# Performance work log

Measured on AMD Instinct MI355X. Metric: run time of the kernel, lower is better.

The kernel has to match this reference:

```python
import jax, jax.numpy as jnp
import numpy as np


def _conv1x1(x, w, b):
    # x: [B,C,H,W], w: [O,C], b: [O] -> [B,O,H,W]
    return jnp.einsum('oc,bchw->bohw', w, x) + b[None, :, None, None]


def setup_inputs() -> dict:
    key = jax.random.key(0)
    ks = jax.random.split(key, 9)
    B, C, O, H, W = 8, 192, 96, 64, 64
    s_in = 1.0 / np.sqrt(C)
    s_out = 1.0 / np.sqrt(O)
    return {
        'x': jax.random.normal(ks[0], (B, C, H, W), dtype=jnp.float32),
        'g_w': jax.random.normal(ks[1], (O, C), dtype=jnp.float32) * s_in,
        'g_b': jax.random.normal(ks[2], (O,), dtype=jnp.float32) * s_in,
        'theta_w': jax.random.normal(ks[3], (O, C), dtype=jnp.float32) * s_in,
        'theta_b': jax.random.normal(ks[4], (O,), dtype=jnp.float32) * s_in,
        'phi_w': jax.random.normal(ks[5], (O, C), dtype=jnp.float32) * s_in,
        'phi_b': jax.random.normal(ks[6], (O,), dtype=jnp.float32) * s_in,
        'W_w': jax.random.normal(ks[7], (C, O), dtype=jnp.float32) * s_out,
        'W_b': jax.random.normal(ks[8], (C,), dtype=jnp.float32) * s_out,
    }


def reference(x, g_w, g_b, theta_w, theta_b, phi_w, phi_b, W_w, W_b):
    B, C, H, W = x.shape
    O = g_w.shape[0]
    N = H * W
    # 1x1 conv projections, flattened to [B, O, N]
    g_x = _conv1x1(x, g_w, g_b).reshape(B, O, N)          # [B,O,N]
    theta_x = _conv1x1(x, theta_w, theta_b).reshape(B, O, N)
    phi_x = _conv1x1(x, phi_w, phi_b).reshape(B, O, N)
    # scores f1[b,n,m] = theta[:, :, n] . phi[:, :, m]
    f1 = jnp.einsum('bon,bom->bnm', theta_x, phi_x)       # [B,N,N]
    f_div_C = jax.nn.softmax(f1, axis=-1)
    # y[b,n,o] = sum_m f[b,n,m] * g[b,o,m]
    y = jnp.einsum('bnm,bom->bon', f_div_C, g_x)          # [B,O,N]
    y = y.reshape(B, O, H, W)
    W_y = _conv1x1(y, W_w, W_b)                           # [B,C,H,W]
    return W_y + x
```

## Files before the change

kernel.cpp:

```cpp
#include <hip/hip_runtime.h>

typedef unsigned short u16;
typedef unsigned int u32;
typedef float f32x4 __attribute__((ext_vector_type(4)));
typedef float f32x16 __attribute__((ext_vector_type(16)));
typedef _Float16 h16x8 __attribute__((ext_vector_type(8)));
typedef u32 u32x4 __attribute__((ext_vector_type(4)));
typedef u32 u32x2 __attribute__((ext_vector_type(2)));
typedef u16 u16x4 __attribute__((ext_vector_type(4)));

#define NB 8
#define CC 192
#define OO 96
#define NN 4096
#define NSPLIT 4
#define XPAD 200
#define LOG2E 1.4426950408889634f

static __device__ __forceinline__ u16 f2h(float f) {
  _Float16 h = (_Float16)f;
  return __builtin_bit_cast(u16, h);
}
static __device__ __forceinline__ void gl_lds16(const u16* g, u16* l) {
  __builtin_amdgcn_global_load_lds(
      (const __attribute__((address_space(1))) void*)g,
      (__attribute__((address_space(3))) void*)l, 16, 0, 0);
}
static __device__ __forceinline__ float exp2_raw(float x) {
  float r;
  asm("v_exp_f32 %0, %1" : "=v"(r) : "v"(x));
  return r;
}
static __device__ __forceinline__ void plane_swap(u32& a, u32& b) {
  u32x2 r = __builtin_amdgcn_permlane32_swap(a, b, false, false);
  a = r[0]; b = r[1];
}
static __device__ __forceinline__ float half_combine_max(float x) {
  u32 a = __builtin_bit_cast(u32, x), b = a;
  plane_swap(a, b);
  return fmaxf(__builtin_bit_cast(float, a), __builtin_bit_cast(float, b));
}
static __device__ __forceinline__ float half_combine_sum(float x) {
  u32 a = __builtin_bit_cast(u32, x), b = a;
  plane_swap(a, b);
  return __builtin_bit_cast(float, a) + __builtin_bit_cast(float, b);
}
static __device__ __forceinline__ float max3f(float a, float b, float c) {
  return fmaxf(fmaxf(a, b), c);
}

__global__ __launch_bounds__(256) void proj_kernel(
    const float* __restrict__ x,
    const float* __restrict__ g_w, const float* __restrict__ g_b,
    const float* __restrict__ th_w, const float* __restrict__ th_b,
    const float* __restrict__ ph_w, const float* __restrict__ ph_b,
    u16* __restrict__ QB, u16* __restrict__ KA, u16* __restrict__ VA)
{
  __shared__ __align__(16) u16 Xs[64][XPAD];
  __shared__ __align__(16) u16 Ws[96][XPAD];
  const int b = blockIdx.y, n0 = blockIdx.x * 64, tid = threadIdx.x;
  const int lane = tid & 63, wv = tid >> 6, l15 = lane & 15, lg = lane >> 4;

  #pragma unroll
  for (int it = 0; it < 12; ++it) {
    int idx = tid + it * 256;
    int c = idx >> 4, q = idx & 15;
    float4 v = *(const float4*)(x + ((size_t)(b * CC + c)) * NN + n0 + q * 4);
    Xs[q * 4 + 0][c] = f2h(v.x); Xs[q * 4 + 1][c] = f2h(v.y);
    Xs[q * 4 + 2][c] = f2h(v.z); Xs[q * 4 + 3][c] = f2h(v.w);
  }

  for (int p = 0; p < 3; ++p) {
    const float* w    = (p == 0) ? th_w : (p == 1) ? ph_w : g_w;
    const float* bias = (p == 0) ? th_b : (p == 1) ? ph_b : g_b;
    const float scale = (p == 0) ? LOG2E : 1.0f;
    __syncthreads();
    #pragma unroll
    for (int it = 0; it < 18; ++it) {
      int idx = tid + it * 256;
      int r = idx / 48, q = idx % 48;
      float4 v = *(const float4*)(w + r * CC + q * 4);
      u16x4 hh; hh[0] = f2h(v.x * scale); hh[1] = f2h(v.y * scale);
      hh[2] = f2h(v.z * scale); hh[3] = f2h(v.w * scale);
      *(u16x4*)&Ws[r][q * 4] = hh;
    }
    __syncthreads();

    f32x4 acc[6];
    #pragma unroll
    for (int of = 0; of < 6; ++of) acc[of] = (f32x4){0.f, 0.f, 0.f, 0.f};
    #pragma unroll
    for (int ks = 0; ks < 6; ++ks) {
      h16x8 xa = *(const h16x8*)&Xs[wv * 16 + l15][ks * 32 + lg * 8];
      #pragma unroll
      for (int of = 0; of < 6; ++of) {
        h16x8 wf = *(const h16x8*)&Ws[of * 16 + l15][ks * 32 + lg * 8];
        if (p < 2) acc[of] = __builtin_amdgcn_mfma_f32_16x16x32_f16(xa, wf, acc[of], 0, 0, 0);
        else       acc[of] = __builtin_amdgcn_mfma_f32_16x16x32_f16(wf, xa, acc[of], 0, 0, 0);
      }
    }

    if (p < 2) {
      u16* dst = (p == 0) ? QB : KA;
      #pragma unroll
      for (int of = 0; of < 6; ++of) {
        int o = of * 16 + l15;
        float bo = bias[o] * scale;
        int kch = of * 2 + (l15 >> 3);
        #pragma unroll
        for (int r = 0; r < 4; ++r) {
          int n = n0 + wv * 16 + lg * 4 + r;
          int idx = (b * 128 + (n >> 5)) * 3072 + (kch * 32 + (n & 31)) * 8 + (o & 7);
          dst[idx] = f2h(acc[of][r] + bo);
        }
      }
    } else {
      #pragma unroll
      for (int of = 0; of < 6; ++of) {
        #pragma unroll
        for (int r = 0; r < 4; ++r) {
          int o = of * 16 + lg * 4 + r;
          int m = n0 + wv * 16 + l15;
          int idx = (b * 256 + (m >> 4)) * 1536 +
                    (((o >> 5) * 2 + ((m >> 3) & 1)) * 32 + (o & 31)) * 8 + (m & 7);
          VA[idx] = f2h(acc[of][r] + bias[o]);
        }
      }
    }
  }
}

static __device__ __forceinline__ void qk_pair(
    const u16* kc, const h16x8* qfA, const h16x8* qfB, int h, int l31,
    f32x16& SA, f32x16& SB)
{
  #pragma unroll
  for (int i = 0; i < 16; ++i) { SA[i] = 0.f; SB[i] = 0.f; }
  #pragma unroll
  for (int ks = 0; ks < 6; ++ks) {
    h16x8 kf = *(const h16x8*)(kc + ((ks * 2 + h) * 32 + l31) * 8);
    SA = __builtin_amdgcn_mfma_f32_32x32x16_f16(kf, qfA[ks], SA, 0, 0, 0);
    SB = __builtin_amdgcn_mfma_f32_32x32x16_f16(kf, qfB[ks], SB, 0, 0, 0);
  }
}

static __device__ __forceinline__ void sm_pair(
    f32x16 SA, f32x16 SB,
    float& mA, float& lA, f32x16* accA,
    float& mB, float& lB, f32x16* accB,
    h16x8* pfA, h16x8* pfB)
{
  float a0 = max3f(SA[0], SA[1], SA[2]),  a1 = max3f(SA[3], SA[4], SA[5]);
  float a2 = max3f(SA[6], SA[7], SA[8]),  a3 = max3f(SA[9], SA[10], SA[11]);
  float a4 = max3f(SA[12], SA[13], SA[14]);
  float pmaxA = half_combine_max(fmaxf(max3f(a0, a1, a2), max3f(a3, a4, SA[15])));
  float b0 = max3f(SB[0], SB[1], SB[2]),  b1 = max3f(SB[3], SB[4], SB[5]);
  float b2 = max3f(SB[6], SB[7], SB[8]),  b3 = max3f(SB[9], SB[10], SB[11]);
  float b4 = max3f(SB[12], SB[13], SB[14]);
  float pmaxB = half_combine_max(fmaxf(max3f(b0, b1, b2), max3f(b3, b4, SB[15])));
  if (__ballot((pmaxA > mA + 11.5416f) || (pmaxB > mB + 11.5416f))) {
    float mnA = fmaxf(mA, pmaxA), scA = exp2_raw(mA - mnA);
    float mnB = fmaxf(mB, pmaxB), scB = exp2_raw(mB - mnB);
    mA = mnA; lA *= scA;
    mB = mnB; lB *= scB;
    #pragma unroll
    for (int ob = 0; ob < 3; ++ob)
      #pragma unroll
      for (int i = 0; i < 16; ++i) { accA[ob][i] *= scA; accB[ob][i] *= scB; }
  }
  #pragma unroll
  for (int i = 0; i < 16; ++i) { SA[i] = exp2_raw(SA[i] - mA); SB[i] = exp2_raw(SB[i] - mB); }
  u32 pkA[8], pkB[8];
  #pragma unroll
  for (int i = 0; i < 8; ++i) {
    pkA[i] = __builtin_bit_cast(u32, __builtin_amdgcn_cvt_pkrtz(SA[2 * i], SA[2 * i + 1]));
    pkB[i] = __builtin_bit_cast(u32, __builtin_amdgcn_cvt_pkrtz(SB[2 * i], SB[2 * i + 1]));
  }
  #pragma unroll
  for (int st = 8; st >= 1; st >>= 1)
    #pragma unroll
    for (int i = 0; i < 8; ++i)
      if (i < st) { SA[i] += SA[i + st]; SB[i] += SB[i + st]; }
  lA += half_combine_sum(SA[0]);
  lB += half_combine_sum(SB[0]);
  plane_swap(pkA[0], pkA[2]); plane_swap(pkA[1], pkA[3]);
  plane_swap(pkA[4], pkA[6]); plane_swap(pkA[5], pkA[7]);
  plane_swap(pkB[0], pkB[2]); plane_swap(pkB[1], pkB[3]);
  plane_swap(pkB[4], pkB[6]); plane_swap(pkB[5], pkB[7]);
  u32x4 a0v = {pkA[0], pkA[1], pkA[2], pkA[3]}, a1v = {pkA[4], pkA[5], pkA[6], pkA[7]};
  u32x4 b0v = {pkB[0], pkB[1], pkB[2], pkB[3]}, b1v = {pkB[4], pkB[5], pkB[6], pkB[7]};
  pfA[0] = __builtin_bit_cast(h16x8, a0v); pfA[1] = __builtin_bit_cast(h16x8, a1v);
  pfB[0] = __builtin_bit_cast(h16x8, b0v); pfB[1] = __builtin_bit_cast(h16x8, b1v);
}

static __device__ __forceinline__ void pv_pair(
    const u16* vc, const h16x8* pfA, const h16x8* pfB, int h, int l31,
    f32x16* accA, f32x16* accB)
{
  #pragma unroll
  for (int s2 = 0; s2 < 2; ++s2) {
    #pragma unroll
    for (int ob = 0; ob < 3; ++ob) {
      h16x8 vf = *(const h16x8*)(vc + (((s2 * 3 + ob) * 2 + h) * 32 + l31) * 8);
      accA[ob] = __builtin_amdgcn_mfma_f32_32x32x16_f16(vf, pfA[s2], accA[ob], 0, 0, 0);
      accB[ob] = __builtin_amdgcn_mfma_f32_32x32x16_f16(vf, pfB[s2], accB[ob], 0, 0, 0);
    }
  }
}

__global__ __launch_bounds__(128, 2) void attn_kernel(
    const u16* __restrict__ QB, const u16* __restrict__ KA,
    const u16* __restrict__ VA, u16* __restrict__ yP, float* __restrict__ ml)
{
  __shared__ __align__(16) u16 Ks[6144];
  __shared__ __align__(16) u16 Vs[6144];
  const int b   = blockIdx.x;
  const int qt  = blockIdx.y;
  const int sp  = blockIdx.z;
  const int tid = threadIdx.x;
  const int lane = tid & 63;
  const int wv  = tid >> 6;
  const int l31 = lane & 31;
  const int h   = lane >> 5;

  const int t_start = 16 * sp;
  const int t_end   = 16 * (sp + 1);

  const int ncA = qt * 4 + wv * 2;
  const int ncB = ncA + 1;
  const u16* qbA = QB + (size_t)(b * 128 + ncA) * 3072;
  const u16* qbB = QB + (size_t)(b * 128 + ncB) * 3072;
  h16x8 qfA[6], qfB[6];
  #pragma unroll
  for (int ks = 0; ks < 6; ++ks) {
    qfA[ks] = *(const h16x8*)(qbA + ((ks * 2 + h) * 32 + l31) * 8);
    qfB[ks] = *(const h16x8*)(qbB + ((ks * 2 + h) * 32 + l31) * 8);
  }

  const u16* gk = KA + (size_t)b * (128 * 3072) + (size_t)t_start * 6144;
  const u16* gv = VA + (size_t)b * (256 * 1536) + (size_t)t_start * 6144;

  f32x16 accA[3], accB[3];
  #pragma unroll
  for (int ob = 0; ob < 3; ++ob)
    #pragma unroll
    for (int i = 0; i < 16; ++i) { accA[ob][i] = 0.f; accB[ob][i] = 0.f; }
  float mA = -3.0e38f, lA = 0.f;
  float mB = -3.0e38f, lB = 0.f;

  for (int t = t_start; t < t_end; ++t) {
    #pragma unroll
    for (int i = 0; i < 6; ++i) gl_lds16(gk + tid * 8 + i * 1024, &Ks[tid * 8 + i * 1024]);
    #pragma unroll
    for (int i = 0; i < 6; ++i) gl_lds16(gv + tid * 8 + i * 1024, &Vs[tid * 8 + i * 1024]);
    gk += 6144; gv += 6144;
    asm volatile("s_waitcnt vmcnt(0)" ::: "memory");
    __builtin_amdgcn_s_barrier();
    __builtin_amdgcn_sched_barrier(0);

    f32x16 SA0, SB0, SA1, SB1;
    h16x8 pfA[2], pfB[2];
    qk_pair(&Ks[0],    qfA, qfB, h, l31, SA0, SB0);
    qk_pair(&Ks[3072], qfA, qfB, h, l31, SA1, SB1);
    sm_pair(SA0, SB0, mA, lA, accA, mB, lB, accB, pfA, pfB);
    pv_pair(&Vs[0], pfA, pfB, h, l31, accA, accB);
    sm_pair(SA1, SB1, mA, lA, accA, mB, lB, accB, pfA, pfB);
    pv_pair(&Vs[3072], pfA, pfB, h, l31, accA, accB);

    __builtin_amdgcn_s_barrier();
  }

  #pragma unroll
  for (int qq = 0; qq < 2; ++qq) {
    const f32x16* acc = qq ? accB : accA;
    float mR = qq ? mB : mA, lR = qq ? lB : lA;
    float inv = 1.0f / lR;
    int nglob = (qq ? ncB : ncA) * 32 + l31;
    u16* yp = yP + (((size_t)sp * NB + b) * NN + nglob) * OO;
    #pragma unroll
    for (int ob = 0; ob < 3; ++ob) {
      #pragma unroll
      for (int rq = 0; rq < 4; ++rq) {
        int o0 = ob * 32 + rq * 8 + h * 4;
        u32 w0 = __builtin_bit_cast(u32,
            __builtin_amdgcn_cvt_pkrtz(acc[ob][rq * 4 + 0] * inv, acc[ob][rq * 4 + 1] * inv));
        u32 w1 = __builtin_bit_cast(u32,
            __builtin_amdgcn_cvt_pkrtz(acc[ob][rq * 4 + 2] * inv, acc[ob][rq * 4 + 3] * inv));
        uint2 pr; pr.x = w0; pr.y = w1;
        *(uint2*)&yp[o0] = pr;
      }
    }
    if (h == 0) {
      float2 v2; v2.x = mR; v2.y = lR;
      *(float2*)&ml[(((size_t)sp * NB + b) * NN + nglob) * 2] = v2;
    }
  }
}

#define YPAD 104
__global__ __launch_bounds__(256) void outproj_kernel(
    const float* __restrict__ x, const float* __restrict__ Ww,
    const float* __restrict__ Wb, const u16* __restrict__ yP,
    const float* __restrict__ ml, float* __restrict__ out)
{
  __shared__ __align__(16) u16 Wws[CC][YPAD];
  __shared__ __align__(16) u16 Ys[64][YPAD];
  const int b = blockIdx.y, n0 = blockIdx.x * 64, tid = threadIdx.x;
  const int lane = tid & 63, wv = tid >> 6, l15 = lane & 15, lg = lane >> 4;
  const size_t SB = (size_t)NB * NN;

  #pragma unroll
  for (int it = 0; it < 18; ++it) {
    int idx = tid + it * 256;
    int r = idx / 24, q = idx % 24;
    float4 v = *(const float4*)(Ww + r * OO + q * 4);
    u16x4 hh; hh[0] = f2h(v.x); hh[1] = f2h(v.y); hh[2] = f2h(v.z); hh[3] = f2h(v.w);
    *(u16x4*)&Wws[r][q * 4] = hh;
  }
  #pragma unroll
  for (int it = 0; it < 3; ++it) {
    int idx = tid + it * 256;
    int n = idx / 12, q = idx % 12;
    size_t bn = (size_t)b * NN + n0 + n;
    float mm[NSPLIT], ll[NSPLIT];
    float M = -3.0e38f;
    #pragma unroll
    for (int s = 0; s < NSPLIT; ++s) {
      mm[s] = ml[((size_t)s * SB + bn) * 2];
      ll[s] = ml[((size_t)s * SB + bn) * 2 + 1];
      M = fmaxf(M, mm[s]);
    }
    float wsum = 0.f, w[NSPLIT];
    #pragma unroll
    for (int s = 0; s < NSPLIT; ++s) { w[s] = ll[s] * exp2f(mm[s] - M); wsum += w[s]; }
    float rinv = 1.0f / wsum;
    #pragma unroll
    for (int s = 0; s < NSPLIT; ++s) w[s] *= rinv;
    float accv[8];
    #pragma unroll
    for (int e = 0; e < 8; ++e) accv[e] = 0.f;
    #pragma unroll
    for (int s = 0; s < NSPLIT; ++s) {
      h16x8 ys = *(const h16x8*)(yP + ((size_t)s * SB + bn) * OO + q * 8);
      #pragma unroll
      for (int e = 0; e < 8; ++e) accv[e] += w[s] * (float)ys[e];
    }
    u32x4 packed;
    #pragma unroll
    for (int e = 0; e < 4; ++e)
      packed[e] = __builtin_bit_cast(u32,
          __builtin_amdgcn_cvt_pkrtz(accv[2 * e], accv[2 * e + 1]));
    *(u32x4*)&Ys[n][q * 8] = packed;
  }
  __syncthreads();

  f32x4 acc[12];
  #pragma unroll
  for (int cf = 0; cf < 12; ++cf) acc[cf] = (f32x4){0.f, 0.f, 0.f, 0.f};
  #pragma unroll
  for (int ks = 0; ks < 3; ++ks) {
    h16x8 yb = *(const h16x8*)&Ys[wv * 16 + l15][ks * 32 + lg * 8];
    #pragma unroll
    for (int cf = 0; cf < 12; ++cf) {
      h16x8 wa = *(const h16x8*)&Wws[cf * 16 + l15][ks * 32 + lg * 8];
      acc[cf] = __builtin_amdgcn_mfma_f32_16x16x32_f16(wa, yb, acc[cf], 0, 0, 0);
    }
  }
  #pragma unroll
  for (int cf = 0; cf < 12; ++cf) {
    #pragma unroll
    for (int r = 0; r < 4; ++r) {
      int c = cf * 16 + lg * 4 + r;
      size_t off = ((size_t)(b * CC + c)) * NN + n0 + wv * 16 + l15;
      out[off] = acc[cf][r] + x[off] + Wb[c];
    }
  }
}

extern "C" void kernel_launch(void* const* d_in, const int* in_sizes, int n_in,
                              void* d_out, int out_size, void* d_ws, size_t ws_size,
                              hipStream_t stream) {
  const float* x    = (const float*)d_in[0];
  const float* g_w  = (const float*)d_in[1];
  const float* g_b  = (const float*)d_in[2];
  const float* th_w = (const float*)d_in[3];
  const float* th_b = (const float*)d_in[4];
  const float* ph_w = (const float*)d_in[5];
  const float* ph_b = (const float*)d_in[6];
  const float* W_w  = (const float*)d_in[7];
  const float* W_b  = (const float*)d_in[8];
  float* out = (float*)d_out;

  char* ws = (char*)d_ws;
  const size_t projB = (size_t)NB * NN * OO * sizeof(u16);
  u16* QB   = (u16*)ws;
  u16* KA   = (u16*)(ws + projB);
  u16* VA   = (u16*)(ws + 2 * projB);
  u16* yP   = (u16*)(ws + 3 * projB);
  float* ml = (float*)(ws + (3 + NSPLIT) * projB);

  dim3 gproj(64, NB);
  hipLaunchKernelGGL(proj_kernel, gproj, dim3(256), 0, stream,
                     x, g_w, g_b, th_w, th_b, ph_w, ph_b, QB, KA, VA);
  dim3 gattn(NB, 32, NSPLIT);
  hipLaunchKernelGGL(attn_kernel, gattn, dim3(128), 0, stream, QB, KA, VA, yP, ml);
  dim3 gout(64, NB);
  hipLaunchKernelGGL(outproj_kernel, gout, dim3(256), 0, stream, x, W_w, W_b, yP, ml, out);
}
```

Before: 97.68 us.

## Double-buffer K/V tiles in LDS and reduce KV split count

Adds a second LDS buffer for the K and V tiles so the next tile's global-to-LDS load is issued right after the barrier and overlaps the current tile's QK, softmax and PV MFMA work. The trailing barrier per iteration is dropped because the buffers now alternate. The KV-sequence split drops from 4 to 3, which gives fewer partial outputs to merge and longer loops per block, but also fewer blocks. LDS use per block doubles, which could lower occupancy, and a split of 3 over 64 tiles gives uneven loop lengths.

Measured after the change: 103.8 us. 6.3% more time.

```diff
diff --git a/kernel.cpp b/kernel.cpp
--- a/kernel.cpp
+++ b/kernel.cpp
@@ -13,7 +13,7 @@
 #define CC 192
 #define OO 96
 #define NN 4096
-#define NSPLIT 4
+#define NSPLIT 3
 #define XPAD 200
 #define LOG2E 1.4426950408889634f
 
@@ -212,8 +212,8 @@
     const u16* __restrict__ QB, const u16* __restrict__ KA,
     const u16* __restrict__ VA, u16* __restrict__ yP, float* __restrict__ ml)
 {
-  __shared__ __align__(16) u16 Ks[6144];
-  __shared__ __align__(16) u16 Vs[6144];
+  __shared__ __align__(16) u16 Ks[2][6144];
+  __shared__ __align__(16) u16 Vs[2][6144];
   const int b   = blockIdx.x;
   const int qt  = blockIdx.y;
   const int sp  = blockIdx.z;
@@ -223,8 +223,8 @@
   const int l31 = lane & 31;
   const int h   = lane >> 5;
 
-  const int t_start = 16 * sp;
-  const int t_end   = 16 * (sp + 1);
+  const int t_start = (64 * sp) / NSPLIT;
+  const int t_end   = (64 * (sp + 1)) / NSPLIT;
 
   const int ncA = qt * 4 + wv * 2;
   const int ncB = ncA + 1;
@@ -237,8 +237,8 @@
     qfB[ks] = *(const h16x8*)(qbB + ((ks * 2 + h) * 32 + l31) * 8);
   }
 
-  const u16* gk = KA + (size_t)b * (128 * 3072) + (size_t)t_start * 6144;
-  const u16* gv = VA + (size_t)b * (256 * 1536) + (size_t)t_start * 6144;
+  const u16* KAb = KA + (size_t)b * (128 * 3072);
+  const u16* VAb = VA + (size_t)b * (256 * 1536);
 
   f32x16 accA[3], accB[3];
   #pragma unroll
@@ -248,26 +248,37 @@
   float mA = -3.0e38f, lA = 0.f;
   float mB = -3.0e38f, lB = 0.f;
 
+  {
+    const u16* gk = KAb + (size_t)t_start * 6144;
+    const u16* gv = VAb + (size_t)t_start * 6144;
+    #pragma unroll
+    for (int i = 0; i < 6; ++i) gl_lds16(gk + tid * 8 + i * 1024, &Ks[0][tid * 8 + i * 1024]);
+    #pragma unroll
+    for (int i = 0; i < 6; ++i) gl_lds16(gv + tid * 8 + i * 1024, &Vs[0][tid * 8 + i * 1024]);
+  }
+
   for (int t = t_start; t < t_end; ++t) {
-    #pragma unroll
-    for (int i = 0; i < 6; ++i) gl_lds16(gk + tid * 8 + i * 1024, &Ks[tid * 8 + i * 1024]);
-    #pragma unroll
-    for (int i = 0; i < 6; ++i) gl_lds16(gv + tid * 8 + i * 1024, &Vs[tid * 8 + i * 1024]);
-    gk += 6144; gv += 6144;
+    const int bf = (t - t_start) & 1;
     asm volatile("s_waitcnt vmcnt(0)" ::: "memory");
     __builtin_amdgcn_s_barrier();
     __builtin_amdgcn_sched_barrier(0);
+    if (t + 1 < t_end) {
+      const u16* gk = KAb + (size_t)(t + 1) * 6144;
+      const u16* gv = VAb + (size_t)(t + 1) * 6144;
+      #pragma unroll
+      for (int i = 0; i < 6; ++i) gl_lds16(gk + tid * 8 + i * 1024, &Ks[bf ^ 1][tid * 8 + i * 1024]);
+      #pragma unroll
+      for (int i = 0; i < 6; ++i) gl_lds16(gv + tid * 8 + i * 1024, &Vs[bf ^ 1][tid * 8 + i * 1024]);
+    }
 
     f32x16 SA0, SB0, SA1, SB1;
     h16x8 pfA[2], pfB[2];
-    qk_pair(&Ks[0],    qfA, qfB, h, l31, SA0, SB0);
-    qk_pair(&Ks[3072], qfA, qfB, h, l31, SA1, SB1);
+    qk_pair(&Ks[bf][0],    qfA, qfB, h, l31, SA0, SB0);
+    qk_pair(&Ks[bf][3072], qfA, qfB, h, l31, SA1, SB1);
     sm_pair(SA0, SB0, mA, lA, accA, mB, lB, accB, pfA, pfB);
-    pv_pair(&Vs[0], pfA, pfB, h, l31, accA, accB);
+    pv_pair(&Vs[bf][0], pfA, pfB, h, l31, accA, accB);
     sm_pair(SA1, SB1, mA, lA, accA, mB, lB, accB, pfA, pfB);
-    pv_pair(&Vs[3072], pfA, pfB, h, l31, accA, accB);
-
-    __builtin_amdgcn_s_barrier();
+    pv_pair(&Vs[bf][3072], pfA, pfB, h, l31, accA, accB);
   }
 
   #pragma unroll
```
